# Kernel tuning notes

Measured on AMD Instinct MI355X. Metric: run time of the kernel, lower is better.

The kernel has to match this reference:

```python
import jax, jax.numpy as jnp
import numpy as np

Q = 128          # number of slices
S = 1024 // Q    # slice length = 8
U = 32           # hidden units per slice
EPS = 1e-3       # keras LayerNormalization default epsilon


def setup_inputs() -> dict:
    key = jax.random.key(0)
    ks = jax.random.split(key, 8)
    B = 16384
    x = jax.random.normal(ks[0], (B, 1, 1, Q * S), dtype=jnp.float32)
    # per-slice Dense1 (S->U), LayerNorm(gamma,beta), Dense2 (U->1)
    W1 = jax.random.normal(ks[1], (Q, S, U), dtype=jnp.float32) / np.sqrt(S)
    b1 = jnp.zeros((Q, U), dtype=jnp.float32)
    gamma = jnp.ones((Q, U), dtype=jnp.float32)
    beta = jnp.zeros((Q, U), dtype=jnp.float32)
    W2 = jax.random.normal(ks[2], (Q, U), dtype=jnp.float32) / np.sqrt(U)
    b2 = jnp.zeros((Q,), dtype=jnp.float32)
    return {"x": x, "W1": W1, "b1": b1, "gamma": gamma, "beta": beta,
            "W2": W2, "b2": b2}


def reference(x, W1, b1, gamma, beta, W2, b2):
    B = x.shape[0]
    xs = x.reshape(B, Q, S)                              # (B,Q,S)
    # batched tiny Dense -> ELU
    h = jnp.einsum('bqs,qsu->bqu', xs, W1) + b1          # (B,Q,U)
    h = jax.nn.elu(h)
    # per-slice LayerNorm over last axis
    mu = jnp.mean(h, axis=-1, keepdims=True)
    var = jnp.mean(jnp.square(h - mu), axis=-1, keepdims=True)
    h = (h - mu) * jax.lax.rsqrt(var + EPS) * gamma + beta
    # batched output projection U -> 1, concat over slices
    out = jnp.einsum('bqu,qu->bq', h, W2) + b2           # (B,Q)
    return out
```

## Files before the change

kernel.cpp:

```cpp
#include <hip/hip_runtime.h>


typedef __attribute__((ext_vector_type(8))) short short8;
typedef __attribute__((ext_vector_type(16))) float f32x16;

__device__ __forceinline__ short fbits(__bf16 b) { return __builtin_bit_cast(short, b); }

__device__ __forceinline__ float elu1(float v) {
    return v > 0.f ? v : __expf(v) - 1.f;
}

__global__ __launch_bounds__(256) void divenc_mfma(
    const float* __restrict__ x,
    const float* __restrict__ W1,
    const float* __restrict__ b1,
    const float* __restrict__ gamma,
    const float* __restrict__ beta,
    const float* __restrict__ W2,
    const float* __restrict__ b2,
    float* __restrict__ out)
{
    __shared__ float lout[2][64 * 5];

    const int tid  = threadIdx.x;
    const int w    = tid >> 6;
    const int ln   = tid & 63;
    const int lo5  = ln & 31;
    const int half = ln >> 5;
    const int qt   = blockIdx.y;
    const int q    = qt * 4 + w;
    const int bx   = blockIdx.x;

    short8 whi = {}, wlo = {};
    if (half == 0) {
        #pragma unroll
        for (int j = 0; j < 8; ++j) {
            float f = W1[q * 256 + j * 32 + lo5];
            __bf16 h = (__bf16)f;
            whi[j] = fbits(h);
            wlo[j] = fbits((__bf16)(f - (float)h));
        }
    }

    f32x16 biasr;
    float g2r[16];
    float G, C;
    {
        float gs = 0.f, cs = 0.f;
        #pragma unroll
        for (int r = 0; r < 16; ++r) {
            int u = (r & 3) + 8 * (r >> 2) + 4 * half;
            float w2 = W2[q * 32 + u];
            g2r[r]   = gamma[q * 32 + u] * w2;
            biasr[r] = b1[q * 32 + u];
            gs += g2r[r];
            cs += beta[q * 32 + u] * w2;
        }
        gs += __shfl_xor(gs, 32);
        cs += __shfl_xor(cs, 32);
        G = gs;
        C = cs + b2[q];
    }

    const float* xq = x + q * 8;

    float4 xa, xb;
    {
        const float* p = xq + (size_t)(bx * 512 + ln) * 1024;
        xa = ((const float4*)p)[0];
        xb = ((const float4*)p)[1];
    }

    #pragma unroll 1
    for (int it = 0; it < 8; ++it) {
        const int b0 = (bx * 8 + it) * 64;

        const int bn = (it < 7) ? b0 + 64 : b0;
        const float* pn = xq + (size_t)(bn + ln) * 1024;
        float4 na = ((const float4*)pn)[0];
        float4 nb = ((const float4*)pn)[1];

        float xf[8] = {xa.x, xa.y, xa.z, xa.w, xb.x, xb.y, xb.z, xb.w};
        short8 xhi, xlo;
        #pragma unroll
        for (int j = 0; j < 8; ++j) {
            __bf16 h = (__bf16)xf[j];
            xhi[j] = fbits(h);
            xlo[j] = fbits((__bf16)(xf[j] - (float)h));
        }

        int4 hI = __builtin_bit_cast(int4, xhi);
        int4 lI = __builtin_bit_cast(int4, xlo);
        int4 h1, l1;
        h1.x = __shfl_xor(hI.x, 32); h1.y = __shfl_xor(hI.y, 32);
        h1.z = __shfl_xor(hI.z, 32); h1.w = __shfl_xor(hI.w, 32);
        l1.x = __shfl_xor(lI.x, 32); l1.y = __shfl_xor(lI.y, 32);
        l1.z = __shfl_xor(lI.z, 32); l1.w = __shfl_xor(lI.w, 32);
        short8 xhi1 = __builtin_bit_cast(short8, h1);
        short8 xlo1 = __builtin_bit_cast(short8, l1);

        f32x16 acc0 = __builtin_amdgcn_mfma_f32_32x32x16_bf16(whi, xhi, biasr, 0, 0, 0);
        acc0 = __builtin_amdgcn_mfma_f32_32x32x16_bf16(whi, xlo, acc0, 0, 0, 0);
        acc0 = __builtin_amdgcn_mfma_f32_32x32x16_bf16(wlo, xhi, acc0, 0, 0, 0);
        f32x16 acc1 = __builtin_amdgcn_mfma_f32_32x32x16_bf16(whi, xhi1, biasr, 0, 0, 0);
        acc1 = __builtin_amdgcn_mfma_f32_32x32x16_bf16(whi, xlo1, acc1, 0, 0, 0);
        acc1 = __builtin_amdgcn_mfma_f32_32x32x16_bf16(wlo, xhi1, acc1, 0, 0, 0);

        float res0, res1;
        {
            float sum = 0.f, ss = 0.f, dot = 0.f;
            #pragma unroll
            for (int r = 0; r < 16; ++r) {
                float e = elu1(acc0[r]);
                sum += e; ss = fmaf(e, e, ss); dot = fmaf(e, g2r[r], dot);
            }
            sum += __shfl_xor(sum, 32);
            ss  += __shfl_xor(ss, 32);
            dot += __shfl_xor(dot, 32);
            float mu  = sum * 0.03125f;
            float var = fmaf(-mu, mu, ss * 0.03125f);
            float inv = rsqrtf(var + 1e-3f);
            res0 = fmaf(inv, fmaf(-mu, G, dot), C);
        }
        {
            float sum = 0.f, ss = 0.f, dot = 0.f;
            #pragma unroll
            for (int r = 0; r < 16; ++r) {
                float e = elu1(acc1[r]);
                sum += e; ss = fmaf(e, e, ss); dot = fmaf(e, g2r[r], dot);
            }
            sum += __shfl_xor(sum, 32);
            ss  += __shfl_xor(ss, 32);
            dot += __shfl_xor(dot, 32);
            float mu  = sum * 0.03125f;
            float var = fmaf(-mu, mu, ss * 0.03125f);
            float inv = rsqrtf(var + 1e-3f);
            res1 = fmaf(inv, fmaf(-mu, G, dot), C);
        }

        lout[it & 1][ln * 5 + w] = half ? res1 : res0;
        __syncthreads();

        if (tid < 64) {
            const float* lb = lout[it & 1];
            float4 o;
            o.x = lb[tid * 5 + 0];
            o.y = lb[tid * 5 + 1];
            o.z = lb[tid * 5 + 2];
            o.w = lb[tid * 5 + 3];
            *(float4*)(out + (size_t)(b0 + tid) * 128 + qt * 4) = o;
        }

        xa = na; xb = nb;
    }
}

extern "C" void kernel_launch(void* const* d_in, const int* in_sizes, int n_in,
                              void* d_out, int out_size, void* d_ws, size_t ws_size,
                              hipStream_t stream) {
    const float* x     = (const float*)d_in[0];
    const float* W1    = (const float*)d_in[1];
    const float* b1    = (const float*)d_in[2];
    const float* gamma = (const float*)d_in[3];
    const float* beta  = (const float*)d_in[4];
    const float* W2    = (const float*)d_in[5];
    const float* b2    = (const float*)d_in[6];
    float* out = (float*)d_out;

    dim3 grid(32, 32);
    divenc_mfma<<<grid, 256, 0, stream>>>(x, W1, b1, gamma, beta, W2, b2, out);
}
```

Measured before the change: 31.43 us.

## Pack W1 hi/lo split into one K=16 MFMA with bf16 x, finer grid

Replaces the three-MFMA hi/lo bf16 emulation per half-wave with a single 32x32x16 MFMA. The K dimension packs the W1 high part (lanes 0-31) and the low residual (lanes 32-63) against the same bf16-rounded x, so the cross-half x shuffles disappear. The b1 and gamma*W2 values move into LDS instead of registers, and each wave now handles 32 batch rows per iteration over 4 iterations, on a 4x larger grid with an occupancy hint. The LDS-staged float4 output store and the barrier are replaced by direct scalar stores. The trade is lower accuracy (x is no longer split into hi/lo) and less coalesced output writes, in exchange for fewer MFMA, convert and shuffle instructions and more parallelism.

```diff
diff --git a/kernel.cpp b/kernel.cpp
--- a/kernel.cpp
+++ b/kernel.cpp
@@ -10,7 +10,7 @@
     return v > 0.f ? v : __expf(v) - 1.f;
 }
 
-__global__ __launch_bounds__(256) void divenc_mfma(
+__global__ __launch_bounds__(256, 8) void divenc_mfma(
     const float* __restrict__ x,
     const float* __restrict__ W1,
     const float* __restrict__ b1,
@@ -20,44 +20,40 @@
     const float* __restrict__ b2,
     float* __restrict__ out)
 {
-    __shared__ float lout[2][64 * 5];
+    __shared__ float lp[4][32][2];
 
     const int tid  = threadIdx.x;
     const int w    = tid >> 6;
     const int ln   = tid & 63;
-    const int lo5  = ln & 31;
+    const int u    = ln & 31;
     const int half = ln >> 5;
     const int qt   = blockIdx.y;
     const int q    = qt * 4 + w;
     const int bx   = blockIdx.x;
 
-    short8 whi = {}, wlo = {};
-    if (half == 0) {
-        #pragma unroll
-        for (int j = 0; j < 8; ++j) {
-            float f = W1[q * 256 + j * 32 + lo5];
-            __bf16 h = (__bf16)f;
-            whi[j] = fbits(h);
-            wlo[j] = fbits((__bf16)(f - (float)h));
-        }
+    short8 wfrag;
+    #pragma unroll
+    for (int j = 0; j < 8; ++j) {
+        float f  = W1[q * 256 + j * 32 + u];
+        __bf16 h = (__bf16)f;
+        wfrag[j] = half ? fbits((__bf16)(f - (float)h)) : fbits(h);
     }
 
-    f32x16 biasr;
-    float g2r[16];
     float G, C;
     {
-        float gs = 0.f, cs = 0.f;
+        float w2 = W2[q * 32 + u];
+        float g2 = gamma[q * 32 + u] * w2;
+        float bw = beta [q * 32 + u] * w2;
+        if (half == 0) {
+            lp[w][u][0] = b1[q * 32 + u];
+            lp[w][u][1] = g2;
+        }
+        float gs = g2, cs = bw;
         #pragma unroll
-        for (int r = 0; r < 16; ++r) {
-            int u = (r & 3) + 8 * (r >> 2) + 4 * half;
-            float w2 = W2[q * 32 + u];
-            g2r[r]   = gamma[q * 32 + u] * w2;
-            biasr[r] = b1[q * 32 + u];
-            gs += g2r[r];
-            cs += beta[q * 32 + u] * w2;
+        for (int m = 1; m < 32; m <<= 1) {
+            gs += __shfl_xor(gs, m);
+            cs += __shfl_xor(cs, m);
         }
-        gs += __shfl_xor(gs, 32);
-        cs += __shfl_xor(cs, 32);
         G = gs;
         C = cs + b2[q];
     }
@@ -66,92 +62,58 @@
 
     float4 xa, xb;
     {
-        const float* p = xq + (size_t)(bx * 512 + ln) * 1024;
+        const float* p = xq + (size_t)(bx * 128 + u) * 1024;
         xa = ((const float4*)p)[0];
         xb = ((const float4*)p)[1];
     }
 
     #pragma unroll 1
-    for (int it = 0; it < 8; ++it) {
-        const int b0 = (bx * 8 + it) * 64;
+    for (int it = 0; it < 4; ++it) {
+        const int b0 = bx * 128 + it * 32;
 
-        const int bn = (it < 7) ? b0 + 64 : b0;
-        const float* pn = xq + (size_t)(bn + ln) * 1024;
+        const int bn = (it < 3) ? b0 + 32 : b0;
+        const float* pn = xq + (size_t)(bn + u) * 1024;
         float4 na = ((const float4*)pn)[0];
         float4 nb = ((const float4*)pn)[1];
 
         float xf[8] = {xa.x, xa.y, xa.z, xa.w, xb.x, xb.y, xb.z, xb.w};
-        short8 xhi, xlo;
+        short8 xfrag;
         #pragma unroll
-        for (int j = 0; j < 8; ++j) {
-            __bf16 h = (__bf16)xf[j];
-            xhi[j] = fbits(h);
-            xlo[j] = fbits((__bf16)(xf[j] - (float)h));
+        for (int j = 0; j < 8; ++j) xfrag[j] = fbits((__bf16)xf[j]);
+
+        f32x16 zacc = {};
+        f32x16 acc = __builtin_amdgcn_mfma_f32_32x32x16_bf16(wfrag, xfrag, zacc, 0, 0, 0);
+
+        float2 sum2 = {0.f, 0.f}, ss2 = {0.f, 0.f}, dot2 = {0.f, 0.f};
+        #pragma unroll
+        for (int r = 0; r < 16; r += 2) {
+            int u0 = (r & 3) + 8 * (r >> 2) + 4 * half;
+            float4 bg = *(const float4*)&lp[w][u0][0];
+            float e0 = elu1(acc[r]     + bg.x);
+            float e1 = elu1(acc[r + 1] + bg.z);
+            sum2.x += e0;
+            sum2.y += e1;
+            ss2.x = fmaf(e0, e0, ss2.x);
+            ss2.y = fmaf(e1, e1, ss2.y);
+            dot2.x = fmaf(e0, bg.y, dot2.x);
+            dot2.y = fmaf(e1, bg.w, dot2.y);
         }
+        float sum = sum2.x + sum2.y;
+        float ss  = ss2.x + ss2.y;
+        float dot = dot2.x + dot2.y;
+        sum += __shfl_xor(sum, 32);
+        ss  += __shfl_xor(ss, 32);
+        dot += __shfl_xor(dot, 32);
+        float mu  = sum * 0.03125f;
+        float var = fmaf(-mu, mu, ss * 0.03125f);
+        float inv = rsqrtf(var + 1e-3f);
+        float res = fmaf(inv, fmaf(-mu, G, dot), C);
 
-        int4 hI = __builtin_bit_cast(int4, xhi);
-        int4 lI = __builtin_bit_cast(int4, xlo);
-        int4 h1, l1;
-        h1.x = __shfl_xor(hI.x, 32); h1.y = __shfl_xor(hI.y, 32);
-        h1.z = __shfl_xor(hI.z, 32); h1.w = __shfl_xor(hI.w, 32);
-        l1.x = __shfl_xor(lI.x, 32); l1.y = __shfl_xor(lI.y, 32);
-        l1.z = __shfl_xor(lI.z, 32); l1.w = __shfl_xor(lI.w, 32);
-        short8 xhi1 = __builtin_bit_cast(short8, h1);
-        short8 xlo1 = __builtin_bit_cast(short8, l1);
+        if (half == 0)
+            out[(size_t)(b0 + u) * 128 + q] = res;
 
-        f32x16 acc0 = __builtin_amdgcn_mfma_f32_32x32x16_bf16(whi, xhi, biasr, 0, 0, 0);
-        acc0 = __builtin_amdgcn_mfma_f32_32x32x16_bf16(whi, xlo, acc0, 0, 0, 0);
-        acc0 = __builtin_amdgcn_mfma_f32_32x32x16_bf16(wlo, xhi, acc0, 0, 0, 0);
-        f32x16 acc1 = __builtin_amdgcn_mfma_f32_32x32x16_bf16(whi, xhi1, biasr, 0, 0, 0);
-        acc1 = __builtin_amdgcn_mfma_f32_32x32x16_bf16(whi, xlo1, acc1, 0, 0, 0);
-        acc1 = __builtin_amdgcn_mfma_f32_32x32x16_bf16(wlo, xhi1, acc1, 0, 0, 0);
-
-        float res0, res1;
-        {
-            float sum = 0.f, ss = 0.f, dot = 0.f;
-            #pragma unroll
-            for (int r = 0; r < 16; ++r) {
-                float e = elu1(acc0[r]);
-                sum += e; ss = fmaf(e, e, ss); dot = fmaf(e, g2r[r], dot);
-            }
-            sum += __shfl_xor(sum, 32);
-            ss  += __shfl_xor(ss, 32);
-            dot += __shfl_xor(dot, 32);
-            float mu  = sum * 0.03125f;
-            float var = fmaf(-mu, mu, ss * 0.03125f);
-            float inv = rsqrtf(var + 1e-3f);
-            res0 = fmaf(inv, fmaf(-mu, G, dot), C);
-        }
-        {
-            float sum = 0.f, ss = 0.f, dot = 0.f;
-            #pragma unroll
-            for (int r = 0; r < 16; ++r) {
-                float e = elu1(acc1[r]);
-                sum += e; ss = fmaf(e, e, ss); dot = fmaf(e, g2r[r], dot);
-            }
-            sum += __shfl_xor(sum, 32);
-            ss  += __shfl_xor(ss, 32);
-            dot += __shfl_xor(dot, 32);
-            float mu  = sum * 0.03125f;
-            float var = fmaf(-mu, mu, ss * 0.03125f);
-            float inv = rsqrtf(var + 1e-3f);
-            res1 = fmaf(inv, fmaf(-mu, G, dot), C);
-        }
-
-        lout[it & 1][ln * 5 + w] = half ? res1 : res0;
-        __syncthreads();
-
-        if (tid < 64) {
-            const float* lb = lout[it & 1];
-            float4 o;
-            o.x = lb[tid * 5 + 0];
-            o.y = lb[tid * 5 + 1];
-            o.z = lb[tid * 5 + 2];
-            o.w = lb[tid * 5 + 3];
-            *(float4*)(out + (size_t)(b0 + tid) * 128 + qt * 4) = o;
-        }
-
-        xa = na; xb = nb;
+        xa = na;
+        xb = nb;
     }
 }
 
@@ -167,6 +129,6 @@
     const float* b2    = (const float*)d_in[6];
     float* out = (float*)d_out;
 
-    dim3 grid(32, 32);
+    dim3 grid(128, 32);
     divenc_mfma<<<grid, 256, 0, stream>>>(x, W1, b1, gamma, beta, W2, b2, out);
 }
```

New measurement: 41.78 us. 32.9% more time.
